# Performance work log

Measured on AMD Instinct MI355X. Metric: run time of the kernel, lower is better.

## Reference

```python
import jax, jax.numpy as jnp
import numpy as np

SIGMA = 0.5  # module's self.sigma (non-learned blend hyperparameter)

def setup_inputs() -> dict:
    key = jax.random.key(0)
    ks = jax.random.split(key, 8)
    B, C, W, H = 8, 256, 64, 64
    Cq = C // 8
    s = 0.02
    return {
        "x": jax.random.normal(ks[0], (B, C, W, H), jnp.float32),
        "Wq": jax.random.normal(ks[1], (Cq, C), jnp.float32) * s,
        "bq": jax.random.normal(ks[2], (Cq,), jnp.float32) * s,
        "Wk": jax.random.normal(ks[3], (Cq, C), jnp.float32) * s,
        "bk": jax.random.normal(ks[4], (Cq,), jnp.float32) * s,
        "Wv": jax.random.normal(ks[5], (C, C), jnp.float32) * s,
        "bv": jax.random.normal(ks[6], (C,), jnp.float32) * s,
        "gamma": jax.random.normal(ks[7], (1,), jnp.float32) * s,
    }

def reference(x, Wq, bq, Wk, bk, Wv, bv, gamma):
    B, C, W, H = x.shape
    N = W * H
    xf = x.reshape(B, C, N)  # flatten spatial
    # 1x1 convs == per-pixel linear projections
    q = jnp.einsum('oc,bcn->bon', Wq, xf) + bq[None, :, None]  # (B, Cq, N)
    k = jnp.einsum('oc,bcn->bon', Wk, xf) + bk[None, :, None]  # (B, Cq, N)
    v = jnp.einsum('oc,bcn->bon', Wv, xf) + bv[None, :, None]  # (B, C, N)
    energy = jnp.einsum('bcn,bcm->bnm', q, k)                  # (B, N, N)
    attention = jax.nn.softmax(energy, axis=-1)
    out = jnp.einsum('bcm,bnm->bcn', v, attention)             # (B, C, N)
    out = out.reshape(B, C, W, H)
    out = gamma[0] * out + x
    out = SIGMA * out + (1.0 - SIGMA) * x
    return out, attention
```

## Files before the change

### kernel.cpp

```cpp
#include <hip/hip_runtime.h>
#include <cstdint>
#include <cstddef>

#define B_ 8
#define C_ 256
#define CQ 32
#define N_ 4096

typedef __attribute__((ext_vector_type(8))) short bf16x8;
typedef __attribute__((ext_vector_type(4))) float f32x4;

__device__ __forceinline__ short f2bf(float f) {
    union { float f; uint32_t u; } v; v.f = f;
    uint32_t r = (v.u + 0x7FFFu + ((v.u >> 16) & 1u)) >> 16;
    return (short)r;
}

__global__ __launch_bounds__(256) void wconv(const float* wq, const float* wk, const float* wv,
                                             short* wqb, short* wkb, short* wvb) {
    int i = blockIdx.x * 256 + threadIdx.x;
    if (i < 8192) { wqb[i] = f2bf(wq[i]); wkb[i] = f2bf(wk[i]); }
    if (i < 65536) wvb[i] = f2bf(wv[i]);
}

__global__ __launch_bounds__(256) void xpose(const float* x, short* xbt) {
    int blk = blockIdx.x;
    int b = blk >> 10;
    int rem = blk & 1023;
    int nt = rem >> 3, ct = rem & 7;
    int n0 = nt * 32, c0 = ct * 32;
    __shared__ short tile[32][33];
    int tx = threadIdx.x & 31, ty = threadIdx.x >> 5;
    const float* xb = x + (size_t)b * C_ * N_;
#pragma unroll
    for (int i = 0; i < 4; i++) {
        int c = c0 + ty + i * 8;
        tile[ty + i * 8][tx] = f2bf(xb[(size_t)c * N_ + n0 + tx]);
    }
    __syncthreads();
    short* dst = xbt + (size_t)b * N_ * C_;
#pragma unroll
    for (int i = 0; i < 4; i++) {
        int n = n0 + ty + i * 8;
        dst[(size_t)n * C_ + c0 + tx] = tile[tx][ty + i * 8];
    }
}

__global__ __launch_bounds__(256) void qkproj(const short* xbt, const short* wqb, const short* wkb,
                                              const float* bq, const float* bk,
                                              short* qt, short* kt) {
    int w = threadIdx.x >> 6, lane = threadIdx.x & 63;
    int gw = blockIdx.x * 4 + w;
    int b = gw >> 8, nt = gw & 255;
    int n0 = nt * 16;
    int col = lane & 15, quad = lane >> 4;
    const bf16x8* arow = (const bf16x8*)(xbt + ((size_t)(b * N_ + n0 + col)) * C_ + quad * 8);
    const bf16x8* q0p = (const bf16x8*)(wqb + (size_t)col * C_ + quad * 8);
    const bf16x8* q1p = (const bf16x8*)(wqb + (size_t)(16 + col) * C_ + quad * 8);
    const bf16x8* k0p = (const bf16x8*)(wkb + (size_t)col * C_ + quad * 8);
    const bf16x8* k1p = (const bf16x8*)(wkb + (size_t)(16 + col) * C_ + quad * 8);
    f32x4 aq0 = {0,0,0,0}, aq1 = {0,0,0,0}, ak0 = {0,0,0,0}, ak1 = {0,0,0,0};
#pragma unroll
    for (int ks = 0; ks < 8; ks++) {
        bf16x8 a = arow[ks * 4];
        aq0 = __builtin_amdgcn_mfma_f32_16x16x32_bf16(a, q0p[ks * 4], aq0, 0, 0, 0);
        aq1 = __builtin_amdgcn_mfma_f32_16x16x32_bf16(a, q1p[ks * 4], aq1, 0, 0, 0);
        ak0 = __builtin_amdgcn_mfma_f32_16x16x32_bf16(a, k0p[ks * 4], ak0, 0, 0, 0);
        ak1 = __builtin_amdgcn_mfma_f32_16x16x32_bf16(a, k1p[ks * 4], ak1, 0, 0, 0);
    }
    float bq0 = bq[col], bq1 = bq[16 + col], bk0 = bk[col], bk1 = bk[16 + col];
#pragma unroll
    for (int r = 0; r < 4; r++) {
        int n = n0 + quad * 4 + r;
        size_t base = ((size_t)b * N_ + n) * CQ;
        qt[base + col]      = f2bf(aq0[r] + bq0);
        qt[base + 16 + col] = f2bf(aq1[r] + bq1);
        kt[base + col]      = f2bf(ak0[r] + bk0);
        kt[base + 16 + col] = f2bf(ak1[r] + bk1);
    }
}

__global__ __launch_bounds__(256) void vproj(const short* xbt, const short* wvb,
                                             const float* bv, short* vb) {
    int w = threadIdx.x >> 6, lane = threadIdx.x & 63;
    int gw = blockIdx.x * 4 + w;
    int b = gw >> 10;
    int rem = gw & 1023;
    int ct = rem >> 6, nt = rem & 63;
    int c0 = ct * 16, n0 = nt * 64;
    int col = lane & 15, quad = lane >> 4;
    const bf16x8* arow = (const bf16x8*)(wvb + (size_t)(c0 + col) * C_ + quad * 8);
    const bf16x8* brow[4];
#pragma unroll
    for (int j = 0; j < 4; j++)
        brow[j] = (const bf16x8*)(xbt + ((size_t)b * N_ + n0 + j * 16 + col) * C_ + quad * 8);
    f32x4 acc[4];
#pragma unroll
    for (int j = 0; j < 4; j++) acc[j] = (f32x4){0,0,0,0};
#pragma unroll
    for (int ks = 0; ks < 8; ks++) {
        bf16x8 a = arow[ks * 4];
#pragma unroll
        for (int j = 0; j < 4; j++)
            acc[j] = __builtin_amdgcn_mfma_f32_16x16x32_bf16(a, brow[j][ks * 4], acc[j], 0, 0, 0);
    }
#pragma unroll
    for (int r = 0; r < 4; r++) {
        int c = c0 + quad * 4 + r;
        float bias = bv[c];
        size_t base = ((size_t)b * C_ + c) * N_ + n0;
#pragma unroll
        for (int j = 0; j < 4; j++)
            vb[base + j * 16 + col] = f2bf(acc[j][r] + bias);
    }
}

__global__ __launch_bounds__(256) void fused_attn(const short* qt, const short* kt,
                                                  const short* vb, const float* x,
                                                  const float* gamma, float* out, float* attn) {
    int blk = blockIdx.x;
    int b = blk >> 6, nt = blk & 63;
    int n0 = nt * 64;
    int t = threadIdx.x;
    int w = t >> 6, lane = t & 63;
    int col = lane & 15, quad = lane >> 4;
    int nw = n0 + w * 16;

    bf16x8 qf = *(const bf16x8*)(qt + ((size_t)(b * N_ + nw + col)) * CQ + quad * 8);
    const short* kbase = kt + (size_t)b * N_ * CQ + quad * 8;

    float mr[4], sr[4];
#pragma unroll
    for (int r = 0; r < 4; r++) { mr[r] = -1e30f; sr[r] = 0.f; }
    for (int m0 = 0; m0 < N_; m0 += 64) {
        f32x4 ev[4];
#pragma unroll
        for (int j = 0; j < 4; j++) {
            bf16x8 kf = *(const bf16x8*)(kbase + (size_t)(m0 + j * 16 + col) * CQ);
            ev[j] = __builtin_amdgcn_mfma_f32_16x16x32_bf16(qf, kf, (f32x4){0,0,0,0}, 0, 0, 0);
        }
#pragma unroll
        for (int r = 0; r < 4; r++) {
            float tm = fmaxf(fmaxf(ev[0][r], ev[1][r]), fmaxf(ev[2][r], ev[3][r]));
            float nm = fmaxf(mr[r], tm);
            sr[r] = sr[r] * __expf(mr[r] - nm)
                  + __expf(ev[0][r] - nm) + __expf(ev[1][r] - nm)
                  + __expf(ev[2][r] - nm) + __expf(ev[3][r] - nm);
            mr[r] = nm;
        }
    }
#pragma unroll
    for (int off = 1; off < 16; off <<= 1) {
#pragma unroll
        for (int r = 0; r < 4; r++) {
            float mo = __shfl_xor(mr[r], off, 64);
            float so = __shfl_xor(sr[r], off, 64);
            float nm = fmaxf(mr[r], mo);
            sr[r] = sr[r] * __expf(mr[r] - nm) + so * __expf(mo - nm);
            mr[r] = nm;
        }
    }
    float inv[4];
#pragma unroll
    for (int r = 0; r < 4; r++) inv[r] = 1.0f / sr[r];

    __shared__ short pl[2][64][72];
    const bf16x8* vrow[4];
#pragma unroll
    for (int i = 0; i < 4; i++)
        vrow[i] = (const bf16x8*)(vb + ((size_t)b * C_ + w * 64 + i * 16 + col) * N_ + quad * 8);
    float* arow[4];
#pragma unroll
    for (int r = 0; r < 4; r++)
        arow[r] = attn + ((size_t)b * N_ + nw + quad * 4 + r) * N_;
    f32x4 acc[4][4];
#pragma unroll
    for (int i = 0; i < 4; i++)
#pragma unroll
        for (int j = 0; j < 4; j++) acc[i][j] = (f32x4){0,0,0,0};

    int par = 0;
    for (int m0 = 0; m0 < N_; m0 += 64) {
        f32x4 ev[4];
#pragma unroll
        for (int j = 0; j < 4; j++) {
            bf16x8 kf = *(const bf16x8*)(kbase + (size_t)(m0 + j * 16 + col) * CQ);
            ev[j] = __builtin_amdgcn_mfma_f32_16x16x32_bf16(qf, kf, (f32x4){0,0,0,0}, 0, 0, 0);
        }
        float pv[4][4];
#pragma unroll
        for (int j = 0; j < 4; j++) {
#pragma unroll
            for (int r = 0; r < 4; r++) {
                float p = __expf(ev[j][r] - mr[r]) * inv[r];
                pv[j][r] = p;
                pl[par][w * 16 + quad * 4 + r][j * 16 + col] = f2bf(p);
            }
        }
        __syncthreads();
#pragma unroll
        for (int j = 0; j < 4; j++)
#pragma unroll
            for (int r = 0; r < 4; r++)
                __builtin_nontemporal_store(pv[j][r], arow[r] + m0 + j * 16 + col);
        bf16x8 bfr[2][4];
#pragma unroll
        for (int kk = 0; kk < 2; kk++)
#pragma unroll
            for (int j = 0; j < 4; j++)
                bfr[kk][j] = *(const bf16x8*)&pl[par][j * 16 + col][kk * 32 + quad * 8];
        int ku = m0 >> 3;
#pragma unroll
        for (int kk = 0; kk < 2; kk++) {
#pragma unroll
            for (int i = 0; i < 4; i++) {
                bf16x8 a = vrow[i][ku + kk * 4];
#pragma unroll
                for (int j = 0; j < 4; j++)
                    acc[i][j] = __builtin_amdgcn_mfma_f32_16x16x32_bf16(a, bfr[kk][j], acc[i][j], 0, 0, 0);
            }
        }
        par ^= 1;
    }

    float g = 0.5f * gamma[0];
#pragma unroll
    for (int i = 0; i < 4; i++) {
#pragma unroll
        for (int r = 0; r < 4; r++) {
            int c = w * 64 + i * 16 + quad * 4 + r;
            size_t base = ((size_t)b * C_ + c) * N_ + n0;
#pragma unroll
            for (int j = 0; j < 4; j++) {
                int n = j * 16 + col;
                float o = g * acc[i][j][r] + x[base + n];
                __builtin_nontemporal_store(o, out + base + n);
            }
        }
    }
}

extern "C" void kernel_launch(void* const* d_in, const int* in_sizes, int n_in,
                              void* d_out, int out_size, void* d_ws, size_t ws_size,
                              hipStream_t stream) {
    const float* x     = (const float*)d_in[0];
    const float* Wq    = (const float*)d_in[1];
    const float* bq    = (const float*)d_in[2];
    const float* Wk    = (const float*)d_in[3];
    const float* bk    = (const float*)d_in[4];
    const float* Wv    = (const float*)d_in[5];
    const float* bv    = (const float*)d_in[6];
    const float* gamma = (const float*)d_in[7];
    float* out  = (float*)d_out;
    float* attn = out + (size_t)B_ * C_ * N_;

    char* ws = (char*)d_ws;
    short* xbt = (short*)(ws);
    short* qt  = (short*)(ws + 16777216);
    short* kt  = (short*)(ws + 18874368);
    short* vb  = (short*)(ws + 20971520);
    short* wqb = (short*)(ws + 37748736);
    short* wkb = (short*)(ws + 37765120);
    short* wvb = (short*)(ws + 37781504);

    hipLaunchKernelGGL(wconv,     dim3(256),  dim3(256), 0, stream, Wq, Wk, Wv, wqb, wkb, wvb);
    hipLaunchKernelGGL(xpose,     dim3(8192), dim3(256), 0, stream, x, xbt);
    hipLaunchKernelGGL(qkproj,    dim3(512),  dim3(256), 0, stream, xbt, wqb, wkb, bq, bk, qt, kt);
    hipLaunchKernelGGL(vproj,     dim3(2048), dim3(256), 0, stream, xbt, wvb, bv, vb);
    hipLaunchKernelGGL(fused_attn,dim3(512),  dim3(256), 0, stream, qt, kt, vb, x, gamma, out, attn);
}
```

Measured before the change: 805.3 us.

## Double attention block warps, stage attn/out through LDS for coalesced vector stores

The fused attention kernel goes from 4 to 8 waves per block. The softmax-statistics pass is split across two halves of the key range, with the partial max and sum merged in shared memory. The fp32 attention probabilities are staged in LDS so each thread writes 32-byte contiguous nontemporal stores instead of scattered scalar stores, and the output epilogue is staged the same way for coalesced x reads and out writes. K fragments are software-prefetched one iteration ahead, and vproj also moves to 512-thread blocks. Costs are more LDS use, extra barriers, and each wave recomputing a share of the QK products.

```diff
diff --git a/kernel.cpp b/kernel.cpp
--- a/kernel.cpp
+++ b/kernel.cpp
@@ -80,14 +80,14 @@
     }
 }
 
-__global__ __launch_bounds__(256) void vproj(const short* xbt, const short* wvb,
+__global__ __launch_bounds__(512) void vproj(const short* xbt, const short* wvb,
                                              const float* bv, short* vb) {
     int w = threadIdx.x >> 6, lane = threadIdx.x & 63;
-    int gw = blockIdx.x * 4 + w;
-    int b = gw >> 10;
-    int rem = gw & 1023;
-    int ct = rem >> 6, nt = rem & 63;
-    int c0 = ct * 16, n0 = nt * 64;
+    int blk = blockIdx.x;
+    int b = blk >> 7;
+    int rem = blk & 127;
+    int ctg = rem >> 6, nt = rem & 63;
+    int c0 = (ctg * 8 + w) * 16, n0 = nt * 64;
     int col = lane & 15, quad = lane >> 4;
     const bf16x8* arow = (const bf16x8*)(wvb + (size_t)(c0 + col) * C_ + quad * 8);
     const bf16x8* brow[4];
@@ -115,7 +115,7 @@
     }
 }
 
-__global__ __launch_bounds__(256) void fused_attn(const short* qt, const short* kt,
+__global__ __launch_bounds__(512) void fused_attn(const short* qt, const short* kt,
                                                   const short* vb, const float* x,
                                                   const float* gamma, float* out, float* attn) {
     int blk = blockIdx.x;
@@ -124,119 +124,156 @@
     int t = threadIdx.x;
     int w = t >> 6, lane = t & 63;
     int col = lane & 15, quad = lane >> 4;
-    int nw = n0 + w * 16;
-
-    bf16x8 qf = *(const bf16x8*)(qt + ((size_t)(b * N_ + nw + col)) * CQ + quad * 8);
+
+    __shared__ float ps[2][64][68];
+    __shared__ short pl[2][64][72];
+    __shared__ float sm[2][2][64];
+
     const short* kbase = kt + (size_t)b * N_ * CQ + quad * 8;
 
-    float mr[4], sr[4];
-#pragma unroll
-    for (int r = 0; r < 4; r++) { mr[r] = -1e30f; sr[r] = 0.f; }
-    for (int m0 = 0; m0 < N_; m0 += 64) {
-        f32x4 ev[4];
-#pragma unroll
-        for (int j = 0; j < 4; j++) {
-            bf16x8 kf = *(const bf16x8*)(kbase + (size_t)(m0 + j * 16 + col) * CQ);
-            ev[j] = __builtin_amdgcn_mfma_f32_16x16x32_bf16(qf, kf, (f32x4){0,0,0,0}, 0, 0, 0);
-        }
-#pragma unroll
-        for (int r = 0; r < 4; r++) {
-            float tm = fmaxf(fmaxf(ev[0][r], ev[1][r]), fmaxf(ev[2][r], ev[3][r]));
-            float nm = fmaxf(mr[r], tm);
-            sr[r] = sr[r] * __expf(mr[r] - nm)
-                  + __expf(ev[0][r] - nm) + __expf(ev[1][r] - nm)
-                  + __expf(ev[2][r] - nm) + __expf(ev[3][r] - nm);
-            mr[r] = nm;
-        }
-    }
-#pragma unroll
-    for (int off = 1; off < 16; off <<= 1) {
-#pragma unroll
-        for (int r = 0; r < 4; r++) {
-            float mo = __shfl_xor(mr[r], off, 64);
-            float so = __shfl_xor(sr[r], off, 64);
-            float nm = fmaxf(mr[r], mo);
-            sr[r] = sr[r] * __expf(mr[r] - nm) + so * __expf(mo - nm);
-            mr[r] = nm;
-        }
-    }
-    float inv[4];
-#pragma unroll
-    for (int r = 0; r < 4; r++) inv[r] = 1.0f / sr[r];
-
-    __shared__ short pl[2][64][72];
-    const bf16x8* vrow[4];
-#pragma unroll
-    for (int i = 0; i < 4; i++)
-        vrow[i] = (const bf16x8*)(vb + ((size_t)b * C_ + w * 64 + i * 16 + col) * N_ + quad * 8);
-    float* arow[4];
-#pragma unroll
-    for (int r = 0; r < 4; r++)
-        arow[r] = attn + ((size_t)b * N_ + nw + quad * 4 + r) * N_;
-    f32x4 acc[4][4];
-#pragma unroll
-    for (int i = 0; i < 4; i++)
-#pragma unroll
-        for (int j = 0; j < 4; j++) acc[i][j] = (f32x4){0,0,0,0};
-
+    {
+        int rw = w & 3, h = w >> 2;
+        bf16x8 qf = *(const bf16x8*)(qt + ((size_t)(b * N_ + n0 + rw * 16 + col)) * CQ + quad * 8);
+        float mr[4], sr[4];
+#pragma unroll
+        for (int r = 0; r < 4; r++) { mr[r] = -1e30f; sr[r] = 0.f; }
+        int mbeg = h * 2048, mend = mbeg + 2048;
+        bf16x8 kf[4];
+#pragma unroll
+        for (int j = 0; j < 4; j++)
+            kf[j] = *(const bf16x8*)(kbase + (size_t)(mbeg + j * 16 + col) * CQ);
+        for (int m0 = mbeg; m0 < mend; m0 += 64) {
+            f32x4 ev[4];
+#pragma unroll
+            for (int j = 0; j < 4; j++)
+                ev[j] = __builtin_amdgcn_mfma_f32_16x16x32_bf16(qf, kf[j], (f32x4){0,0,0,0}, 0, 0, 0);
+            int mn = m0 + 64;
+#pragma unroll
+            for (int j = 0; j < 4; j++)
+                kf[j] = *(const bf16x8*)(kbase + (size_t)(mn + j * 16 + col) * CQ);
+#pragma unroll
+            for (int r = 0; r < 4; r++) {
+                float tm = fmaxf(fmaxf(ev[0][r], ev[1][r]), fmaxf(ev[2][r], ev[3][r]));
+                float nm = fmaxf(mr[r], tm);
+                sr[r] = sr[r] * __expf(mr[r] - nm)
+                      + __expf(ev[0][r] - nm) + __expf(ev[1][r] - nm)
+                      + __expf(ev[2][r] - nm) + __expf(ev[3][r] - nm);
+                mr[r] = nm;
+            }
+        }
+#pragma unroll
+        for (int off = 1; off < 16; off <<= 1) {
+#pragma unroll
+            for (int r = 0; r < 4; r++) {
+                float mo = __shfl_xor(mr[r], off, 64);
+                float so = __shfl_xor(sr[r], off, 64);
+                float nm = fmaxf(mr[r], mo);
+                sr[r] = sr[r] * __expf(mr[r] - nm) + so * __expf(mo - nm);
+                mr[r] = nm;
+            }
+        }
+        if (col == 0) {
+#pragma unroll
+            for (int r = 0; r < 4; r++) {
+                int rr = rw * 16 + quad * 4 + r;
+                sm[0][h][rr] = mr[r];
+                sm[1][h][rr] = sr[r];
+            }
+        }
+    }
+    __syncthreads();
+    if (t < 64) {
+        float ma = sm[0][0][t], mb = sm[0][1][t];
+        float M = fmaxf(ma, mb);
+        float S = sm[1][0][t] * __expf(ma - M) + sm[1][1][t] * __expf(mb - M);
+        sm[0][0][t] = M;
+        sm[1][0][t] = 1.0f / S;
+    }
+    __syncthreads();
+
+    int it = w >> 1, jb = (w & 1) * 2;
+    float mrow[4], irow[4];
+#pragma unroll
+    for (int r = 0; r < 4; r++) {
+        int rr = it * 16 + quad * 4 + r;
+        mrow[r] = sm[0][0][rr];
+        irow[r] = sm[1][0][rr];
+    }
+    bf16x8 qf2 = *(const bf16x8*)(qt + ((size_t)(b * N_ + n0 + it * 16 + col)) * CQ + quad * 8);
+    const bf16x8* vrowp[2];
+#pragma unroll
+    for (int i2 = 0; i2 < 2; i2++)
+        vrowp[i2] = (const bf16x8*)(vb + ((size_t)b * C_ + w * 32 + i2 * 16 + col) * N_ + quad * 8);
+    int srow = t >> 3, sch = t & 7;
+    float* abase = attn + ((size_t)b * N_ + n0 + srow) * N_ + sch * 8;
+    f32x4 acc[2][4];
+#pragma unroll
+    for (int i2 = 0; i2 < 2; i2++)
+#pragma unroll
+        for (int j = 0; j < 4; j++) acc[i2][j] = (f32x4){0,0,0,0};
+
+    bf16x8 kfa = *(const bf16x8*)(kbase + (size_t)(jb * 16 + col) * CQ);
+    bf16x8 kfb = *(const bf16x8*)(kbase + (size_t)(jb * 16 + 16 + col) * CQ);
     int par = 0;
     for (int m0 = 0; m0 < N_; m0 += 64) {
-        f32x4 ev[4];
-#pragma unroll
-        for (int j = 0; j < 4; j++) {
-            bf16x8 kf = *(const bf16x8*)(kbase + (size_t)(m0 + j * 16 + col) * CQ);
-            ev[j] = __builtin_amdgcn_mfma_f32_16x16x32_bf16(qf, kf, (f32x4){0,0,0,0}, 0, 0, 0);
-        }
-        float pv[4][4];
-#pragma unroll
-        for (int j = 0; j < 4; j++) {
-#pragma unroll
-            for (int r = 0; r < 4; r++) {
-                float p = __expf(ev[j][r] - mr[r]) * inv[r];
-                pv[j][r] = p;
-                pl[par][w * 16 + quad * 4 + r][j * 16 + col] = f2bf(p);
+        f32x4 eva = __builtin_amdgcn_mfma_f32_16x16x32_bf16(qf2, kfa, (f32x4){0,0,0,0}, 0, 0, 0);
+        f32x4 evb = __builtin_amdgcn_mfma_f32_16x16x32_bf16(qf2, kfb, (f32x4){0,0,0,0}, 0, 0, 0);
+        int mn = m0 + 64;
+        kfa = *(const bf16x8*)(kbase + (size_t)(mn + jb * 16 + col) * CQ);
+        kfb = *(const bf16x8*)(kbase + (size_t)(mn + jb * 16 + 16 + col) * CQ);
+#pragma unroll
+        for (int r = 0; r < 4; r++) {
+            int rr = it * 16 + quad * 4 + r;
+            float pa = __expf(eva[r] - mrow[r]) * irow[r];
+            float pb = __expf(evb[r] - mrow[r]) * irow[r];
+            ps[par][rr][jb * 16 + col]      = pa;
+            ps[par][rr][jb * 16 + 16 + col] = pb;
+            pl[par][rr][jb * 16 + col]      = f2bf(pa);
+            pl[par][rr][jb * 16 + 16 + col] = f2bf(pb);
+        }
+        __syncthreads();
+        f32x4 s0 = *(const f32x4*)&ps[par][srow][sch * 8];
+        f32x4 s1 = *(const f32x4*)&ps[par][srow][sch * 8 + 4];
+        __builtin_nontemporal_store(s0, (f32x4*)(abase + m0));
+        __builtin_nontemporal_store(s1, (f32x4*)(abase + m0 + 4));
+        int ku = m0 >> 3;
+#pragma unroll
+        for (int kk = 0; kk < 2; kk++) {
+            bf16x8 bfr[4];
+#pragma unroll
+            for (int jn = 0; jn < 4; jn++)
+                bfr[jn] = *(const bf16x8*)&pl[par][jn * 16 + col][kk * 32 + quad * 8];
+#pragma unroll
+            for (int i2 = 0; i2 < 2; i2++) {
+                bf16x8 a = vrowp[i2][ku + kk * 4];
+#pragma unroll
+                for (int jn = 0; jn < 4; jn++)
+                    acc[i2][jn] = __builtin_amdgcn_mfma_f32_16x16x32_bf16(a, bfr[jn], acc[i2][jn], 0, 0, 0);
             }
         }
+        par ^= 1;
+    }
+
+    float g = 0.5f * gamma[0];
+    for (int g4 = 0; g4 < 4; g4++) {
+        if ((w >> 1) == g4) {
+#pragma unroll
+            for (int i2 = 0; i2 < 2; i2++)
+#pragma unroll
+                for (int jn = 0; jn < 4; jn++)
+#pragma unroll
+                    for (int r = 0; r < 4; r++)
+                        ps[0][(w & 1) * 32 + i2 * 16 + quad * 4 + r][jn * 16 + col] = g * acc[i2][jn][r];
+        }
         __syncthreads();
-#pragma unroll
-        for (int j = 0; j < 4; j++)
-#pragma unroll
-            for (int r = 0; r < 4; r++)
-                __builtin_nontemporal_store(pv[j][r], arow[r] + m0 + j * 16 + col);
-        bf16x8 bfr[2][4];
-#pragma unroll
-        for (int kk = 0; kk < 2; kk++)
-#pragma unroll
-            for (int j = 0; j < 4; j++)
-                bfr[kk][j] = *(const bf16x8*)&pl[par][j * 16 + col][kk * 32 + quad * 8];
-        int ku = m0 >> 3;
-#pragma unroll
-        for (int kk = 0; kk < 2; kk++) {
-#pragma unroll
-            for (int i = 0; i < 4; i++) {
-                bf16x8 a = vrow[i][ku + kk * 4];
-#pragma unroll
-                for (int j = 0; j < 4; j++)
-                    acc[i][j] = __builtin_amdgcn_mfma_f32_16x16x32_bf16(a, bfr[kk][j], acc[i][j], 0, 0, 0);
-            }
-        }
-        par ^= 1;
-    }
-
-    float g = 0.5f * gamma[0];
-#pragma unroll
-    for (int i = 0; i < 4; i++) {
-#pragma unroll
-        for (int r = 0; r < 4; r++) {
-            int c = w * 64 + i * 16 + quad * 4 + r;
-            size_t base = ((size_t)b * C_ + c) * N_ + n0;
-#pragma unroll
-            for (int j = 0; j < 4; j++) {
-                int n = j * 16 + col;
-                float o = g * acc[i][j][r] + x[base + n];
-                __builtin_nontemporal_store(o, out + base + n);
-            }
-        }
+        size_t base = ((size_t)b * C_ + g4 * 64 + srow) * N_ + n0 + sch * 8;
+        f32x4 o0 = *(const f32x4*)&ps[0][srow][sch * 8];
+        f32x4 o1 = *(const f32x4*)&ps[0][srow][sch * 8 + 4];
+        f32x4 x0 = *(const f32x4*)(x + base);
+        f32x4 x1 = *(const f32x4*)(x + base + 4);
+        __builtin_nontemporal_store(o0 + x0, (f32x4*)(out + base));
+        __builtin_nontemporal_store(o1 + x1, (f32x4*)(out + base + 4));
+        __syncthreads();
     }
 }
 
@@ -266,6 +303,6 @@
     hipLaunchKernelGGL(wconv,     dim3(256),  dim3(256), 0, stream, Wq, Wk, Wv, wqb, wkb, wvb);
     hipLaunchKernelGGL(xpose,     dim3(8192), dim3(256), 0, stream, x, xbt);
     hipLaunchKernelGGL(qkproj,    dim3(512),  dim3(256), 0, stream, xbt, wqb, wkb, bq, bk, qt, kt);
-    hipLaunchKernelGGL(vproj,     dim3(2048), dim3(256), 0, stream, xbt, wvb, bv, vb);
-    hipLaunchKernelGGL(fused_attn,dim3(512),  dim3(256), 0, stream, qt, kt, vb, x, gamma, out, attn);
-}
+    hipLaunchKernelGGL(vproj,     dim3(1024), dim3(512), 0, stream, xbt, wvb, bv, vb);
+    hipLaunchKernelGGL(fused_attn,dim3(512),  dim3(512), 0, stream, qt, kt, vb, x, gamma, out, attn);
+}
```

Measured after the change: 909.6 us. 13.0% more time.
